# Kernel tuning notes

Measured on AMD Instinct MI355X. Metric: run time of the kernel, lower is better.

The kernel has to match this reference:

```python
import jax, jax.numpy as jnp
import numpy as np

EPS = 1e-5

def rmsnorm(x, weight, eps=EPS):
    var = jnp.mean(x * x, axis=-1, keepdims=True)
    return x * jax.lax.rsqrt(var + eps) * weight

def activation_quant(x):
    # per-token absmax int8 quantization (BitNet b1.58)
    scale = 127.0 / jnp.clip(jnp.max(jnp.abs(x), axis=-1, keepdims=True), 1e-5, None)
    return jnp.clip(jnp.round(x * scale), -128, 127) / scale

def weight_quant(w):
    # ternary absmean quantization
    scale = 1.0 / jnp.clip(jnp.mean(jnp.abs(w)), 1e-5, None)
    return jnp.clip(jnp.round(w * scale), -1, 1) / scale

def bitlinear(x, w):
    # forward math of BitLinear (STE only matters for backward)
    xq = activation_quant(x)
    wq = weight_quant(w)
    return jnp.einsum('bsh,oh->bso', xq, wq)

def setup_inputs() -> dict:
    key = jax.random.key(0)
    k1, k2, k3 = jax.random.split(key, 3)
    B, S, H, F = 4, 2048, 2048, 5632
    x = jax.random.normal(k1, (B, S, H), dtype=jnp.float32)
    w_gate_up = jax.random.normal(k2, (2 * F, H), dtype=jnp.float32) * 0.02
    w_down = jax.random.normal(k3, (H, F), dtype=jnp.float32) * 0.02
    norm_weight = jnp.ones((H,), dtype=jnp.float32)
    return {"x": x, "w_gate_up": w_gate_up, "w_down": w_down, "norm_weight": norm_weight}

def reference(x, w_gate_up, w_down, norm_weight):
    x_norm = rmsnorm(x, norm_weight)
    gate_up = bitlinear(x_norm, w_gate_up)          # [B,S,2F]
    gate, up = jnp.split(gate_up, 2, axis=-1)
    hidden = jnp.square(jax.nn.relu(gate)) * up      # relu(gate)**2 * up
    return bitlinear(hidden, w_down)                 # [B,S,H]
```

## Files before the change

### kernel.cpp

```cpp
#include <hip/hip_runtime.h>
#include <stdint.h>

typedef __attribute__((ext_vector_type(4))) float f32x4;
typedef __attribute__((ext_vector_type(4))) int i32x4;

#define ROWS  8192
#define H     2048
#define F     5632
#define N1    11264
#define NW1   23068672
#define NW2   11534336

__device__ __forceinline__ void gload16(const void* g, void* l) {
  __builtin_amdgcn_global_load_lds((const __attribute__((address_space(1))) void*)g,
                                   (__attribute__((address_space(3))) void*)l, 16, 0, 0);
}

__global__ void leaf_abs(const float* __restrict__ w, float* __restrict__ leaves) {
  int L = blockIdx.x * 256 + threadIdx.x;
  const f32x4* a4 = (const f32x4*)(w + (size_t)L * 88);
  f32x4 u0 = a4[0], u1 = a4[1];
  float r0 = fabsf(u0.x), r1 = fabsf(u0.y), r2 = fabsf(u0.z), r3 = fabsf(u0.w);
  float r4 = fabsf(u1.x), r5 = fabsf(u1.y), r6 = fabsf(u1.z), r7 = fabsf(u1.w);
  #pragma unroll
  for (int it = 1; it <= 10; ++it) {
    f32x4 p0 = a4[2*it], p1 = a4[2*it+1];
    r0 = __fadd_rn(r0, fabsf(p0.x)); r1 = __fadd_rn(r1, fabsf(p0.y));
    r2 = __fadd_rn(r2, fabsf(p0.z)); r3 = __fadd_rn(r3, fabsf(p0.w));
    r4 = __fadd_rn(r4, fabsf(p1.x)); r5 = __fadd_rn(r5, fabsf(p1.y));
    r6 = __fadd_rn(r6, fabsf(p1.z)); r7 = __fadd_rn(r7, fabsf(p1.w));
  }
  leaves[L] = __fadd_rn(__fadd_rn(__fadd_rn(r0,r1), __fadd_rn(r2,r3)),
                        __fadd_rn(__fadd_rn(r4,r5), __fadd_rn(r6,r7)));
}

__global__ void tree_l1(const float* __restrict__ leaves, float* __restrict__ partials) {
  __shared__ float sm[256];
  int tid = threadIdx.x;
  const float* b = leaves + (size_t)blockIdx.x * 1024 + (size_t)tid * 4;
  sm[tid] = __fadd_rn(__fadd_rn(b[0], b[1]), __fadd_rn(b[2], b[3]));
  __syncthreads();
  for (int s = 1; s < 256; s <<= 1) {
    if ((tid & (2*s-1)) == 0) sm[tid] = __fadd_rn(sm[tid], sm[tid+s]);
    __syncthreads();
  }
  if (tid == 0) partials[blockIdx.x] = sm[0];
}

__global__ void tree_final(const float* __restrict__ p1, const float* __restrict__ p2,
                           double* __restrict__ dsc, float* __restrict__ fsc) {
  __shared__ float sm[256];
  __shared__ float tot1s;
  int tid = threadIdx.x;
  sm[tid] = p1[tid];
  __syncthreads();
  for (int s = 1; s < 256; s <<= 1) {
    if ((tid & (2*s-1)) == 0) sm[tid] = __fadd_rn(sm[tid], sm[tid+s]);
    __syncthreads();
  }
  if (tid == 0) tot1s = sm[0];
  __syncthreads();
  sm[tid] = (tid < 128) ? p2[tid] : 0.0f;
  __syncthreads();
  for (int s = 1; s < 256; s <<= 1) {
    if ((tid & (2*s-1)) == 0) sm[tid] = __fadd_rn(sm[tid], sm[tid+s]);
    __syncthreads();
  }
  if (tid == 0) {
    float tot2 = sm[0];
    float mean1 = (float)((double)tot1s / (double)NW1);
    float mean2 = (float)((double)tot2  / (double)NW2);
    mean2 = __uint_as_float(__float_as_uint(mean2) + 1u);
    float m1c = fmaxf(mean1, 1e-5f), m2c = fmaxf(mean2, 1e-5f);
    float sc1 = __fdiv_rn(1.0f, m1c);
    float sc2 = __fdiv_rn(1.0f, m2c);
    fsc[0] = sc1; fsc[1] = sc2;
    dsc[0] = (double)sc1;
    dsc[1] = (double)__fdiv_rn(1.0f, sc1);
    dsc[2] = (double)sc2;
    dsc[3] = (double)__fdiv_rn(1.0f, sc2);
  }
}

__device__ __forceinline__ int qw32(float x, float sc) {
  float r = rintf(__fmul_rn(x, sc));
  r = fminf(fmaxf(r, -1.0f), 1.0f);
  return (int)r;
}
__device__ __forceinline__ int qa32(float x, float sc) {
  float r = rintf(__fmul_rn(x, sc));
  r = fminf(fmaxf(r, -128.0f), 127.0f);
  return (int)r;
}

__global__ void quant_wgu(const float* __restrict__ w, int8_t* __restrict__ q,
                          const float* __restrict__ fsc) {
  float sc = fsc[0];
  int t = blockIdx.x * 256 + threadIdx.x;
  int row = t >> 9;
  int k4 = (t & 511) << 2;
  f32x4 v = *(const f32x4*)(w + ((size_t)row << 11) + k4);
  int nr = (row < F) ? (row << 1) : (((row - F) << 1) | 1);
  int b0 = qw32(v.x, sc), b1 = qw32(v.y, sc), b2 = qw32(v.z, sc), b3 = qw32(v.w, sc);
  unsigned pk = (b0 & 255) | ((b1 & 255) << 8) | ((b2 & 255) << 16) | ((b3 & 255) << 24);
  *(unsigned*)(q + ((size_t)nr << 11) + k4) = pk;
}

__global__ void quant_wd(const float* __restrict__ w, int8_t* __restrict__ q,
                         const float* __restrict__ fsc) {
  float sc = fsc[1];
  int t = blockIdx.x * 256 + threadIdx.x;
  int row = t / 1408;
  int k4 = (t - row * 1408) << 2;
  size_t off = (size_t)row * F + k4;
  f32x4 v = *(const f32x4*)(w + off);
  int b0 = qw32(v.x, sc), b1 = qw32(v.y, sc), b2 = qw32(v.z, sc), b3 = qw32(v.w, sc);
  unsigned pk = (b0 & 255) | ((b1 & 255) << 8) | ((b2 & 255) << 16) | ((b3 & 255) << 24);
  *(unsigned*)(q + off) = pk;
}

__launch_bounds__(256)
__global__ void rms_quant(const float* __restrict__ x, const float* __restrict__ nw,
                          int8_t* __restrict__ xq, double* __restrict__ ax) {
  int row = blockIdx.x, tid = threadIdx.x;
  const float* xr = x + ((size_t)row << 11);
  __shared__ float lsm[16];
  __shared__ float sm[4];
  __shared__ float bc;
  if (tid < 16) {
    const f32x4* a4 = (const f32x4*)(xr + tid * 128);
    f32x4 u0 = a4[0], u1 = a4[1];
    float r0 = __fmul_rn(u0.x,u0.x), r1 = __fmul_rn(u0.y,u0.y);
    float r2 = __fmul_rn(u0.z,u0.z), r3 = __fmul_rn(u0.w,u0.w);
    float r4 = __fmul_rn(u1.x,u1.x), r5 = __fmul_rn(u1.y,u1.y);
    float r6 = __fmul_rn(u1.z,u1.z), r7 = __fmul_rn(u1.w,u1.w);
    #pragma unroll
    for (int it = 1; it <= 15; ++it) {
      f32x4 p0 = a4[2*it], p1 = a4[2*it+1];
      r0 = __fadd_rn(r0, __fmul_rn(p0.x,p0.x)); r1 = __fadd_rn(r1, __fmul_rn(p0.y,p0.y));
      r2 = __fadd_rn(r2, __fmul_rn(p0.z,p0.z)); r3 = __fadd_rn(r3, __fmul_rn(p0.w,p0.w));
      r4 = __fadd_rn(r4, __fmul_rn(p1.x,p1.x)); r5 = __fadd_rn(r5, __fmul_rn(p1.y,p1.y));
      r6 = __fadd_rn(r6, __fmul_rn(p1.z,p1.z)); r7 = __fadd_rn(r7, __fmul_rn(p1.w,p1.w));
    }
    lsm[tid] = __fadd_rn(__fadd_rn(__fadd_rn(r0,r1), __fadd_rn(r2,r3)),
                         __fadd_rn(__fadd_rn(r4,r5), __fadd_rn(r6,r7)));
  }
  __syncthreads();
  if (tid == 0) {
    float q0 = __fadd_rn(lsm[0],lsm[1]),  q1 = __fadd_rn(lsm[2],lsm[3]);
    float q2 = __fadd_rn(lsm[4],lsm[5]),  q3 = __fadd_rn(lsm[6],lsm[7]);
    float q4 = __fadd_rn(lsm[8],lsm[9]),  q5 = __fadd_rn(lsm[10],lsm[11]);
    float q6 = __fadd_rn(lsm[12],lsm[13]), q7 = __fadd_rn(lsm[14],lsm[15]);
    float h0 = __fadd_rn(q0,q1), h1 = __fadd_rn(q2,q3);
    float h2 = __fadd_rn(q4,q5), h3 = __fadd_rn(q6,q7);
    float s = __fadd_rn(__fadd_rn(h0,h1), __fadd_rn(h2,h3));
    float varm = (float)((double)s / 2048.0);
    bc = __fdiv_rn(1.0f, __fsqrt_rn(__fadd_rn(varm, 1e-5f)));
  }
  __syncthreads();
  float rstd = bc;
  f32x4 v0 = *(const f32x4*)(xr + tid * 8);
  f32x4 v1 = *(const f32x4*)(xr + tid * 8 + 4);
  f32x4 w0 = *(const f32x4*)(nw + tid * 8);
  f32x4 w1 = *(const f32x4*)(nw + tid * 8 + 4);
  float xv[8] = {v0.x,v0.y,v0.z,v0.w,v1.x,v1.y,v1.z,v1.w};
  float wv[8] = {w0.x,w0.y,w0.z,w0.w,w1.x,w1.y,w1.z,w1.w};
  float xn[8];
  float am = 0.f;
  #pragma unroll
  for (int j = 0; j < 8; ++j) {
    xn[j] = __fmul_rn(__fmul_rn(xv[j], rstd), wv[j]);
    am = fmaxf(am, fabsf(xn[j]));
  }
  int lane = tid & 63, wid = tid >> 6;
  for (int off = 32; off; off >>= 1) am = fmaxf(am, __shfl_down(am, off));
  if (lane == 0) sm[wid] = am;
  __syncthreads();
  if (tid == 0) {
    float amax = fmaxf(fmaxf(sm[0], sm[1]), fmaxf(sm[2], sm[3]));
    float sc = __fdiv_rn(127.0f, fmaxf(amax, 1e-5f));
    bc = sc;
    ax[row] = 1.0 / (double)sc;
  }
  __syncthreads();
  float sc = bc;
  int q[8];
  #pragma unroll
  for (int j = 0; j < 8; ++j) q[j] = qa32(xn[j], sc);
  int2 pk;
  pk.x = (q[0] & 255) | ((q[1] & 255) << 8) | ((q[2] & 255) << 16) | ((q[3] & 255) << 24);
  pk.y = (q[4] & 255) | ((q[5] & 255) << 8) | ((q[6] & 255) << 16) | ((q[7] & 255) << 24);
  *(int2*)(xq + ((size_t)row << 11) + tid * 8) = pk;
}

__launch_bounds__(512)
__global__ void hid_quant(const float* __restrict__ h,
                          int8_t* __restrict__ hq, double* __restrict__ ah) {
  int row = blockIdx.x, tid = threadIdx.x;
  __shared__ float rowbuf[F];
  __shared__ float sm[8];
  __shared__ float bc;
  const float* hr = h + (size_t)row * F;
  float am = 0.f;
  for (int i = tid * 4; i < F; i += 2048) {
    f32x4 v = *(const f32x4*)(hr + i);
    *(f32x4*)(rowbuf + i) = v;
    am = fmaxf(am, fmaxf(fmaxf(fabsf(v.x), fabsf(v.y)), fmaxf(fabsf(v.z), fabsf(v.w))));
  }
  int lane = tid & 63, wid = tid >> 6;
  for (int off = 32; off; off >>= 1) am = fmaxf(am, __shfl_down(am, off));
  if (lane == 0) sm[wid] = am;
  __syncthreads();
  if (tid == 0) {
    float amax = fmaxf(fmaxf(fmaxf(sm[0], sm[1]), fmaxf(sm[2], sm[3])),
                       fmaxf(fmaxf(sm[4], sm[5]), fmaxf(sm[6], sm[7])));
    amax = fmaxf(amax, 1e-5f);
    float sc = __fdiv_rn(127.0f, amax);
    bc = sc;
    ah[row] = 1.0 / (double)sc;
  }
  __syncthreads();
  float sc = bc;
  int8_t* qr = hq + (size_t)row * F;
  for (int i = tid * 4; i < F; i += 2048) {
    float vx = rowbuf[i], vy = rowbuf[i+1], vz = rowbuf[i+2], vw = rowbuf[i+3];
    int b0 = qa32(vx, sc), b1 = qa32(vy, sc), b2 = qa32(vz, sc), b3 = qa32(vw, sc);
    unsigned pk = (b0 & 255) | ((b1 & 255) << 8) | ((b2 & 255) << 16) | ((b3 & 255) << 24);
    *(unsigned*)(qr + i) = pk;
  }
}

template <bool GATEUP, int TNC>
__launch_bounds__(512, 2)
__global__ void gemm_i8(const int8_t* __restrict__ A, const int8_t* __restrict__ B,
                        int K, const double* __restrict__ arow,
                        const double* __restrict__ dsc, int dqidx,
                        float* __restrict__ outp, int ldo) {
  __shared__ __align__(16) int8_t lsA[4][256 * 64];
  __shared__ __align__(16) int8_t lsB[4][256 * 64];
  int tid = threadIdx.x, wid = tid >> 6, lane = tid & 63;
  int cpx = gridDim.x >> 3;
  int nid = (blockIdx.x & 7) * cpx + (blockIdx.x >> 3);
  int m0 = (nid / TNC) * 256, n0 = (nid % TNC) * 256;
  int wr = wid >> 2, wc = wid & 3;
  i32x4 acc[8][4] = {};
  double dq = dsc[dqidx];
  int nk = K >> 6;
  int schunk = (lane & 3) ^ ((lane >> 3) & 3);
  const int8_t* aS = A + (size_t)(m0 + wid * 16 + (lane >> 2)) * K + (schunk << 4);
  const int8_t* bS = B + (size_t)(n0 + wid * 16 + (lane >> 2)) * K + (schunk << 4);
  size_t hstep = (size_t)128 * K;
  int rl = lane & 15;
  int ksw = (((lane >> 4) ^ ((rl >> 1) & 3)) << 4);

  #define STAGE_A(t,h) gload16(aS + (size_t)(t)*64 + (size_t)(h)*hstep, \
                               &lsA[(t)&3][((h)*128 + wid*16)*64])
  #define STAGE_B(t,h) gload16(bS + (size_t)(t)*64 + (size_t)(h)*hstep, \
                               &lsB[(t)&3][((h)*128 + wid*16)*64])

  STAGE_A(0,0); STAGE_B(0,0); STAGE_A(0,1); STAGE_B(0,1);
  STAGE_A(1,0); STAGE_B(1,0); STAGE_A(1,1); STAGE_B(1,1);
  STAGE_A(2,0); STAGE_B(2,0); STAGE_A(2,1); STAGE_B(2,1);
  asm volatile("s_waitcnt vmcnt(8)" ::: "memory");
  __builtin_amdgcn_s_barrier();

  for (int t = 0; t < nk; ++t) {
    const int8_t* bufA = lsA[t & 3];
    const int8_t* bufB = lsB[t & 3];
    bool pf = (t + 3 < nk);
    i32x4 a[8], b[4];
    #pragma unroll
    for (int m = 0; m < 4; ++m)
      a[m] = *(const i32x4*)&bufA[(wr * 128 + m * 16 + rl) * 64 + ksw];
    #pragma unroll
    for (int n = 0; n < 4; ++n)
      b[n] = *(const i32x4*)&bufB[(wc * 64 + n * 16 + rl) * 64 + ksw];
    if (pf) { STAGE_A(t + 3, 0); STAGE_A(t + 3, 1); }
    __builtin_amdgcn_s_barrier();
    __builtin_amdgcn_s_setprio(1);
    #pragma unroll
    for (int m = 0; m < 4; ++m)
      #pragma unroll
      for (int n = 0; n < 4; ++n)
        acc[m][n] = __builtin_amdgcn_mfma_i32_16x16x64_i8(a[m], b[n], acc[m][n], 0, 0, 0);
    __builtin_amdgcn_s_setprio(0);
    __builtin_amdgcn_s_barrier();
    #pragma unroll
    for (int m = 4; m < 8; ++m)
      a[m] = *(const i32x4*)&bufA[(wr * 128 + m * 16 + rl) * 64 + ksw];
    if (pf) { STAGE_B(t + 3, 0); STAGE_B(t + 3, 1); }
    if (t + 3 < nk)      asm volatile("s_waitcnt vmcnt(8)" ::: "memory");
    else if (t + 2 < nk) asm volatile("s_waitcnt vmcnt(4)" ::: "memory");
    else if (t + 1 < nk) asm volatile("s_waitcnt vmcnt(0)" ::: "memory");
    __builtin_amdgcn_s_barrier();
    __builtin_amdgcn_s_setprio(1);
    #pragma unroll
    for (int m = 4; m < 8; ++m)
      #pragma unroll
      for (int n = 0; n < 4; ++n)
        acc[m][n] = __builtin_amdgcn_mfma_i32_16x16x64_i8(a[m], b[n], acc[m][n], 0, 0, 0);
    __builtin_amdgcn_s_setprio(0);
    __builtin_amdgcn_s_barrier();
  }
  #undef STAGE_A
  #undef STAGE_B

  int rb0 = m0 + wr * 128 + ((lane >> 4) << 2);
  #pragma unroll
  for (int m = 0; m < 8; ++m) {
    double arv[4];
    #pragma unroll
    for (int j = 0; j < 4; ++j)
      arv[j] = arow[rb0 + m * 16 + j] * dq;
    if (GATEUP) {
      #pragma unroll
      for (int n = 0; n < 4; ++n) {
        int icol = n0 + wc * 64 + n * 16 + rl;
        #pragma unroll
        for (int j = 0; j < 4; ++j) {
          float vf = (float)((double)acc[m][n][j] * arv[j]);
          float of = __shfl_xor(vf, 1);
          if (!(lane & 1)) {
            float g = fmaxf(vf, 0.0f);
            float hh = __fmul_rn(__fmul_rn(g, g), of);
            outp[(size_t)(rb0 + m * 16 + j) * ldo + (icol >> 1)] = hh;
          }
        }
      }
    } else {
      #pragma unroll
      for (int n = 0; n < 4; ++n) {
        int col = n0 + wc * 64 + n * 16 + rl;
        #pragma unroll
        for (int j = 0; j < 4; ++j)
          outp[(size_t)(rb0 + m * 16 + j) * ldo + col] = (float)((double)acc[m][n][j] * arv[j]);
      }
    }
  }
}

extern "C" void kernel_launch(void* const* d_in, const int* in_sizes, int n_in,
                              void* d_out, int out_size, void* d_ws, size_t ws_size,
                              hipStream_t stream) {
  (void)in_sizes; (void)n_in; (void)out_size; (void)ws_size;
  const float* x   = (const float*)d_in[0];
  const float* wgu = (const float*)d_in[1];
  const float* wd  = (const float*)d_in[2];
  const float* nw  = (const float*)d_in[3];
  float* out = (float*)d_out;

  char* p = (char*)d_ws;
  double*   dsc     = (double*)(p + 0);
  float*    fsc     = (float*)(p + 64);
  float*    part1   = (float*)(p + 128);
  float*    part2   = (float*)(p + 1152);
  float*    leaves1 = (float*)(p + 2048);
  float*    leaves2 = (float*)(p + 1050624);
  double*   ax      = (double*)(p + 1574912);
  double*   ah      = (double*)(p + 1640448);
  int8_t*   xq      = (int8_t*)(p + 2097152);
  int8_t*   wqg     = (int8_t*)(p + 18874368);
  int8_t*   wqd     = (int8_t*)(p + 41943040);
  int8_t*   hq      = (int8_t*)(p + 53477376);
  float*    hidden  = (float*)(p + 99614720);

  leaf_abs<<<1024, 256, 0, stream>>>(wgu, leaves1);
  leaf_abs<<<512,  256, 0, stream>>>(wd,  leaves2);
  tree_l1<<<256, 256, 0, stream>>>(leaves1, part1);
  tree_l1<<<128, 256, 0, stream>>>(leaves2, part2);
  tree_final<<<1, 256, 0, stream>>>(part1, part2, dsc, fsc);
  quant_wgu<<<NW1 / 4 / 256, 256, 0, stream>>>(wgu, wqg, fsc);
  quant_wd<<<NW2 / 4 / 256, 256, 0, stream>>>(wd, wqd, fsc);
  rms_quant<<<ROWS, 256, 0, stream>>>(x, nw, xq, ax);
  gemm_i8<true, 44><<<(ROWS / 256) * (N1 / 256), 512, 0, stream>>>(
      xq, wqg, H, ax, dsc, 1, hidden, F);
  hid_quant<<<ROWS, 512, 0, stream>>>(hidden, hq, ah);
  gemm_i8<false, 8><<<(ROWS / 256) * (H / 256), 512, 0, stream>>>(
      hq, wqd, F, ah, dsc, 3, out, H);
}
```

Baseline: 482.6 us.

## Double-buffer B fragments in registers and cut barriers in int8 GEMM loop

Rewrites the int8 MFMA GEMM main loop as a two-way unrolled body. The B fragments for the next k-step are prefetched into a second register set while the current step's MFMAs run. All global-to-LDS prefetches for stage t+3 are issued at once, with a single vmcnt wait and two barriers per k-step instead of four. This is meant to cut synchronisation stalls and hide LDS read latency behind MFMA work. The cost is higher register pressure from the extra B fragment set, and the loop now assumes an even k-step count.

```diff
diff --git a/kernel.cpp b/kernel.cpp
--- a/kernel.cpp
+++ b/kernel.cpp
@@ -230,6 +230,47 @@
   }
 }
 
+#define ITER_BODY(T, BCUR, BNXT)                                              \
+  {                                                                           \
+    if ((T) + 3 < nk) {                                                       \
+      STAGE_A((T)+3,0); STAGE_A((T)+3,1); STAGE_B((T)+3,0); STAGE_B((T)+3,1); \
+      asm volatile("s_waitcnt vmcnt(4)" ::: "memory");                        \
+    } else if ((T) + 2 < nk) {                                                \
+      asm volatile("s_waitcnt vmcnt(0)" ::: "memory");                        \
+    }                                                                         \
+    __builtin_amdgcn_s_barrier();                                             \
+    const int8_t* bufA_ = lsA[(T) & 3];                                       \
+    const int8_t* bufB1_ = lsB[((T) + 1) & 3];                                \
+    _Pragma("unroll")                                                         \
+    for (int m = 0; m < 4; ++m)                                               \
+      a[m] = *(const i32x4*)&bufA_[(wr * 128 + m * 16 + rl) * 64 + ksw];      \
+    __builtin_amdgcn_s_setprio(1);                                            \
+    _Pragma("unroll")                                                         \
+    for (int m = 0; m < 4; ++m)                                               \
+      _Pragma("unroll")                                                       \
+      for (int n = 0; n < 4; ++n)                                             \
+        acc[m][n] = __builtin_amdgcn_mfma_i32_16x16x64_i8(a[m], BCUR[n],      \
+                                                          acc[m][n], 0, 0, 0);\
+    __builtin_amdgcn_s_setprio(0);                                            \
+    _Pragma("unroll")                                                         \
+    for (int m = 4; m < 8; ++m)                                               \
+      a[m] = *(const i32x4*)&bufA_[(wr * 128 + m * 16 + rl) * 64 + ksw];      \
+    if ((T) + 1 < nk) {                                                       \
+      _Pragma("unroll")                                                       \
+      for (int n = 0; n < 4; ++n)                                             \
+        BNXT[n] = *(const i32x4*)&bufB1_[(wc * 64 + n * 16 + rl) * 64 + ksw]; \
+    }                                                                         \
+    __builtin_amdgcn_s_setprio(1);                                            \
+    _Pragma("unroll")                                                         \
+    for (int m = 4; m < 8; ++m)                                               \
+      _Pragma("unroll")                                                       \
+      for (int n = 0; n < 4; ++n)                                             \
+        acc[m][n] = __builtin_amdgcn_mfma_i32_16x16x64_i8(a[m], BCUR[n],      \
+                                                          acc[m][n], 0, 0, 0);\
+    __builtin_amdgcn_s_setprio(0);                                            \
+    __builtin_amdgcn_s_barrier();                                             \
+  }
+
 template <bool GATEUP, int TNC>
 __launch_bounds__(512, 2)
 __global__ void gemm_i8(const int8_t* __restrict__ A, const int8_t* __restrict__ B,
@@ -261,46 +302,17 @@
   STAGE_A(0,0); STAGE_B(0,0); STAGE_A(0,1); STAGE_B(0,1);
   STAGE_A(1,0); STAGE_B(1,0); STAGE_A(1,1); STAGE_B(1,1);
   STAGE_A(2,0); STAGE_B(2,0); STAGE_A(2,1); STAGE_B(2,1);
-  asm volatile("s_waitcnt vmcnt(8)" ::: "memory");
+  asm volatile("s_waitcnt vmcnt(4)" ::: "memory");
   __builtin_amdgcn_s_barrier();
 
-  for (int t = 0; t < nk; ++t) {
-    const int8_t* bufA = lsA[t & 3];
-    const int8_t* bufB = lsB[t & 3];
-    bool pf = (t + 3 < nk);
-    i32x4 a[8], b[4];
-    #pragma unroll
-    for (int m = 0; m < 4; ++m)
-      a[m] = *(const i32x4*)&bufA[(wr * 128 + m * 16 + rl) * 64 + ksw];
-    #pragma unroll
-    for (int n = 0; n < 4; ++n)
-      b[n] = *(const i32x4*)&bufB[(wc * 64 + n * 16 + rl) * 64 + ksw];
-    if (pf) { STAGE_A(t + 3, 0); STAGE_A(t + 3, 1); }
-    __builtin_amdgcn_s_barrier();
-    __builtin_amdgcn_s_setprio(1);
-    #pragma unroll
-    for (int m = 0; m < 4; ++m)
-      #pragma unroll
-      for (int n = 0; n < 4; ++n)
-        acc[m][n] = __builtin_amdgcn_mfma_i32_16x16x64_i8(a[m], b[n], acc[m][n], 0, 0, 0);
-    __builtin_amdgcn_s_setprio(0);
-    __builtin_amdgcn_s_barrier();
-    #pragma unroll
-    for (int m = 4; m < 8; ++m)
-      a[m] = *(const i32x4*)&bufA[(wr * 128 + m * 16 + rl) * 64 + ksw];
-    if (pf) { STAGE_B(t + 3, 0); STAGE_B(t + 3, 1); }
-    if (t + 3 < nk)      asm volatile("s_waitcnt vmcnt(8)" ::: "memory");
-    else if (t + 2 < nk) asm volatile("s_waitcnt vmcnt(4)" ::: "memory");
-    else if (t + 1 < nk) asm volatile("s_waitcnt vmcnt(0)" ::: "memory");
-    __builtin_amdgcn_s_barrier();
-    __builtin_amdgcn_s_setprio(1);
-    #pragma unroll
-    for (int m = 4; m < 8; ++m)
-      #pragma unroll
-      for (int n = 0; n < 4; ++n)
-        acc[m][n] = __builtin_amdgcn_mfma_i32_16x16x64_i8(a[m], b[n], acc[m][n], 0, 0, 0);
-    __builtin_amdgcn_s_setprio(0);
-    __builtin_amdgcn_s_barrier();
+  i32x4 a[8], bA[4], bB[4];
+  #pragma unroll
+  for (int n = 0; n < 4; ++n)
+    bA[n] = *(const i32x4*)&lsB[0][(wc * 64 + n * 16 + rl) * 64 + ksw];
+
+  for (int t = 0; t < nk; t += 2) {
+    ITER_BODY(t,     bA, bB)
+    ITER_BODY(t + 1, bB, bA)
   }
   #undef STAGE_A
   #undef STAGE_B
```

New measurement: 556.9 us. +15.4%, slower.

## Shrink int8 GEMM tiles to 128x128 with 256-thread blocks

Applied to the files above, without the earlier changes.

The int8 GEMM tile drops from 256x256 with 8 waves to 128x128 with 4 waves. Each wave keeps a 64x64 accumulator, LDS per block shrinks to a quarter, and the grid grows to four times as many blocks. The split-phase A/B prefetch schedule is merged into one phase per k-step with a single barrier pair. This may raise occupancy and improve wave balance across CUs, but each block reuses its loaded data less, so global and LDS traffic per MFMA goes up.

```diff
diff --git a/kernel.cpp b/kernel.cpp
--- a/kernel.cpp
+++ b/kernel.cpp
@@ -231,51 +231,55 @@
 }
 
 template <bool GATEUP, int TNC>
-__launch_bounds__(512, 2)
+__launch_bounds__(256, 2)
 __global__ void gemm_i8(const int8_t* __restrict__ A, const int8_t* __restrict__ B,
                         int K, const double* __restrict__ arow,
                         const double* __restrict__ dsc, int dqidx,
                         float* __restrict__ outp, int ldo) {
-  __shared__ __align__(16) int8_t lsA[4][256 * 64];
-  __shared__ __align__(16) int8_t lsB[4][256 * 64];
+  __shared__ __align__(16) int8_t lsA[4][128 * 64];
+  __shared__ __align__(16) int8_t lsB[4][128 * 64];
   int tid = threadIdx.x, wid = tid >> 6, lane = tid & 63;
   int cpx = gridDim.x >> 3;
   int nid = (blockIdx.x & 7) * cpx + (blockIdx.x >> 3);
-  int m0 = (nid / TNC) * 256, n0 = (nid % TNC) * 256;
-  int wr = wid >> 2, wc = wid & 3;
-  i32x4 acc[8][4] = {};
+  int m0 = (nid / TNC) * 128, n0 = (nid % TNC) * 128;
+  int wr = wid >> 1, wc = wid & 1;
+  i32x4 acc[4][4] = {};
   double dq = dsc[dqidx];
   int nk = K >> 6;
   int schunk = (lane & 3) ^ ((lane >> 3) & 3);
   const int8_t* aS = A + (size_t)(m0 + wid * 16 + (lane >> 2)) * K + (schunk << 4);
   const int8_t* bS = B + (size_t)(n0 + wid * 16 + (lane >> 2)) * K + (schunk << 4);
-  size_t hstep = (size_t)128 * K;
+  size_t hstep = (size_t)64 * K;
   int rl = lane & 15;
   int ksw = (((lane >> 4) ^ ((rl >> 1) & 3)) << 4);
 
   #define STAGE_A(t,h) gload16(aS + (size_t)(t)*64 + (size_t)(h)*hstep, \
-                               &lsA[(t)&3][((h)*128 + wid*16)*64])
+                               &lsA[(t)&3][((h)*64 + wid*16)*64])
   #define STAGE_B(t,h) gload16(bS + (size_t)(t)*64 + (size_t)(h)*hstep, \
-                               &lsB[(t)&3][((h)*128 + wid*16)*64])
-
-  STAGE_A(0,0); STAGE_B(0,0); STAGE_A(0,1); STAGE_B(0,1);
-  STAGE_A(1,0); STAGE_B(1,0); STAGE_A(1,1); STAGE_B(1,1);
-  STAGE_A(2,0); STAGE_B(2,0); STAGE_A(2,1); STAGE_B(2,1);
+                               &lsB[(t)&3][((h)*64 + wid*16)*64])
+
+  STAGE_A(0,0); STAGE_A(0,1); STAGE_B(0,0); STAGE_B(0,1);
+  STAGE_A(1,0); STAGE_A(1,1); STAGE_B(1,0); STAGE_B(1,1);
+  STAGE_A(2,0); STAGE_A(2,1); STAGE_B(2,0); STAGE_B(2,1);
   asm volatile("s_waitcnt vmcnt(8)" ::: "memory");
   __builtin_amdgcn_s_barrier();
 
   for (int t = 0; t < nk; ++t) {
     const int8_t* bufA = lsA[t & 3];
     const int8_t* bufB = lsB[t & 3];
-    bool pf = (t + 3 < nk);
-    i32x4 a[8], b[4];
+    i32x4 a[4], b[4];
     #pragma unroll
     for (int m = 0; m < 4; ++m)
-      a[m] = *(const i32x4*)&bufA[(wr * 128 + m * 16 + rl) * 64 + ksw];
+      a[m] = *(const i32x4*)&bufA[(wr * 64 + m * 16 + rl) * 64 + ksw];
     #pragma unroll
     for (int n = 0; n < 4; ++n)
       b[n] = *(const i32x4*)&bufB[(wc * 64 + n * 16 + rl) * 64 + ksw];
-    if (pf) { STAGE_A(t + 3, 0); STAGE_A(t + 3, 1); }
+    if (t + 3 < nk) {
+      STAGE_A(t+3,0); STAGE_A(t+3,1); STAGE_B(t+3,0); STAGE_B(t+3,1);
+      asm volatile("s_waitcnt vmcnt(8)" ::: "memory");
+    } else if (t + 2 < nk) {
+      asm volatile("s_waitcnt vmcnt(0)" ::: "memory");
+    }
     __builtin_amdgcn_s_barrier();
     __builtin_amdgcn_s_setprio(1);
     #pragma unroll
@@ -285,29 +289,13 @@
         acc[m][n] = __builtin_amdgcn_mfma_i32_16x16x64_i8(a[m], b[n], acc[m][n], 0, 0, 0);
     __builtin_amdgcn_s_setprio(0);
     __builtin_amdgcn_s_barrier();
-    #pragma unroll
-    for (int m = 4; m < 8; ++m)
-      a[m] = *(const i32x4*)&bufA[(wr * 128 + m * 16 + rl) * 64 + ksw];
-    if (pf) { STAGE_B(t + 3, 0); STAGE_B(t + 3, 1); }
-    if (t + 3 < nk)      asm volatile("s_waitcnt vmcnt(8)" ::: "memory");
-    else if (t + 2 < nk) asm volatile("s_waitcnt vmcnt(4)" ::: "memory");
-    else if (t + 1 < nk) asm volatile("s_waitcnt vmcnt(0)" ::: "memory");
-    __builtin_amdgcn_s_barrier();
-    __builtin_amdgcn_s_setprio(1);
-    #pragma unroll
-    for (int m = 4; m < 8; ++m)
-      #pragma unroll
-      for (int n = 0; n < 4; ++n)
-        acc[m][n] = __builtin_amdgcn_mfma_i32_16x16x64_i8(a[m], b[n], acc[m][n], 0, 0, 0);
-    __builtin_amdgcn_s_setprio(0);
-    __builtin_amdgcn_s_barrier();
   }
   #undef STAGE_A
   #undef STAGE_B
 
-  int rb0 = m0 + wr * 128 + ((lane >> 4) << 2);
+  int rb0 = m0 + wr * 64 + ((lane >> 4) << 2);
   #pragma unroll
-  for (int m = 0; m < 8; ++m) {
+  for (int m = 0; m < 4; ++m) {
     double arv[4];
     #pragma unroll
     for (int j = 0; j < 4; ++j)
@@ -372,9 +360,9 @@
   quant_wgu<<<NW1 / 4 / 256, 256, 0, stream>>>(wgu, wqg, fsc);
   quant_wd<<<NW2 / 4 / 256, 256, 0, stream>>>(wd, wqd, fsc);
   rms_quant<<<ROWS, 256, 0, stream>>>(x, nw, xq, ax);
-  gemm_i8<true, 44><<<(ROWS / 256) * (N1 / 256), 512, 0, stream>>>(
+  gemm_i8<true, 88><<<(ROWS / 128) * (N1 / 128), 256, 0, stream>>>(
       xq, wqg, H, ax, dsc, 1, hidden, F);
   hid_quant<<<ROWS, 512, 0, stream>>>(hidden, hq, ah);
-  gemm_i8<false, 8><<<(ROWS / 256) * (H / 256), 512, 0, stream>>>(
+  gemm_i8<false, 16><<<(ROWS / 128) * (H / 128), 256, 0, stream>>>(
       hq, wqd, F, ah, dsc, 3, out, H);
 }
```

Result: slower. 549.7 us (+13.9%).

## Restructure int8 GEMM main loop to stage two K-tiles per barrier pair

Applied to the files above, without the earlier changes.

The K loop now steps two tiles at a time. Each iteration issues the global-to-LDS loads for the next two tiles, waits, and hits one barrier. It then runs all 8x4 MFMAs for two tiles back to back. The earlier version split each tile into half-A phases with four barriers per tile and a three-deep prefetch. The aim is to cut barrier count and the interleaving overhead. In exchange, prefetch distance drops to two tiles with two in flight, so load latency is less well hidden, and more A fragments are live in registers at once.

```diff
diff --git a/kernel.cpp b/kernel.cpp
--- a/kernel.cpp
+++ b/kernel.cpp
@@ -253,57 +253,61 @@
   int rl = lane & 15;
   int ksw = (((lane >> 4) ^ ((rl >> 1) & 3)) << 4);
 
-  #define STAGE_A(t,h) gload16(aS + (size_t)(t)*64 + (size_t)(h)*hstep, \
-                               &lsA[(t)&3][((h)*128 + wid*16)*64])
-  #define STAGE_B(t,h) gload16(bS + (size_t)(t)*64 + (size_t)(h)*hstep, \
-                               &lsB[(t)&3][((h)*128 + wid*16)*64])
-
-  STAGE_A(0,0); STAGE_B(0,0); STAGE_A(0,1); STAGE_B(0,1);
-  STAGE_A(1,0); STAGE_B(1,0); STAGE_A(1,1); STAGE_B(1,1);
-  STAGE_A(2,0); STAGE_B(2,0); STAGE_A(2,1); STAGE_B(2,1);
-  asm volatile("s_waitcnt vmcnt(8)" ::: "memory");
-  __builtin_amdgcn_s_barrier();
-
-  for (int t = 0; t < nk; ++t) {
-    const int8_t* bufA = lsA[t & 3];
-    const int8_t* bufB = lsB[t & 3];
-    bool pf = (t + 3 < nk);
-    i32x4 a[8], b[4];
-    #pragma unroll
-    for (int m = 0; m < 4; ++m)
-      a[m] = *(const i32x4*)&bufA[(wr * 128 + m * 16 + rl) * 64 + ksw];
-    #pragma unroll
-    for (int n = 0; n < 4; ++n)
-      b[n] = *(const i32x4*)&bufB[(wc * 64 + n * 16 + rl) * 64 + ksw];
-    if (pf) { STAGE_A(t + 3, 0); STAGE_A(t + 3, 1); }
+  #define STAGE_T(t) { \
+    gload16(aS + (size_t)(t)*64,         &lsA[(t)&3][(wid*16)*64]);        \
+    gload16(aS + (size_t)(t)*64 + hstep, &lsA[(t)&3][(128 + wid*16)*64]);  \
+    gload16(bS + (size_t)(t)*64,         &lsB[(t)&3][(wid*16)*64]);        \
+    gload16(bS + (size_t)(t)*64 + hstep, &lsB[(t)&3][(128 + wid*16)*64]); }
+
+  STAGE_T(0); STAGE_T(1);
+
+  for (int t = 0; t < nk; t += 2) {
+    if (t + 2 < nk) {
+      STAGE_T(t + 2); STAGE_T(t + 3);
+      asm volatile("s_waitcnt vmcnt(8)" ::: "memory");
+    } else {
+      asm volatile("s_waitcnt vmcnt(0)" ::: "memory");
+    }
     __builtin_amdgcn_s_barrier();
-    __builtin_amdgcn_s_setprio(1);
-    #pragma unroll
-    for (int m = 0; m < 4; ++m)
+    {
+      const int8_t* bufA = lsA[t & 3];
+      const int8_t* bufB = lsB[t & 3];
+      i32x4 a[8], b[4];
+      #pragma unroll
+      for (int m = 0; m < 8; ++m)
+        a[m] = *(const i32x4*)&bufA[(wr * 128 + m * 16 + rl) * 64 + ksw];
       #pragma unroll
       for (int n = 0; n < 4; ++n)
-        acc[m][n] = __builtin_amdgcn_mfma_i32_16x16x64_i8(a[m], b[n], acc[m][n], 0, 0, 0);
-    __builtin_amdgcn_s_setprio(0);
+        b[n] = *(const i32x4*)&bufB[(wc * 64 + n * 16 + rl) * 64 + ksw];
+      __builtin_amdgcn_s_setprio(1);
+      #pragma unroll
+      for (int m = 0; m < 8; ++m)
+        #pragma unroll
+        for (int n = 0; n < 4; ++n)
+          acc[m][n] = __builtin_amdgcn_mfma_i32_16x16x64_i8(a[m], b[n], acc[m][n], 0, 0, 0);
+      __builtin_amdgcn_s_setprio(0);
+    }
+    {
+      const int8_t* bufA = lsA[(t + 1) & 3];
+      const int8_t* bufB = lsB[(t + 1) & 3];
+      i32x4 a[8], b[4];
+      #pragma unroll
+      for (int m = 0; m < 8; ++m)
+        a[m] = *(const i32x4*)&bufA[(wr * 128 + m * 16 + rl) * 64 + ksw];
+      #pragma unroll
+      for (int n = 0; n < 4; ++n)
+        b[n] = *(const i32x4*)&bufB[(wc * 64 + n * 16 + rl) * 64 + ksw];
+      __builtin_amdgcn_s_setprio(1);
+      #pragma unroll
+      for (int m = 0; m < 8; ++m)
+        #pragma unroll
+        for (int n = 0; n < 4; ++n)
+          acc[m][n] = __builtin_amdgcn_mfma_i32_16x16x64_i8(a[m], b[n], acc[m][n], 0, 0, 0);
+      __builtin_amdgcn_s_setprio(0);
+    }
     __builtin_amdgcn_s_barrier();
-    #pragma unroll
-    for (int m = 4; m < 8; ++m)
-      a[m] = *(const i32x4*)&bufA[(wr * 128 + m * 16 + rl) * 64 + ksw];
-    if (pf) { STAGE_B(t + 3, 0); STAGE_B(t + 3, 1); }
-    if (t + 3 < nk)      asm volatile("s_waitcnt vmcnt(8)" ::: "memory");
-    else if (t + 2 < nk) asm volatile("s_waitcnt vmcnt(4)" ::: "memory");
-    else if (t + 1 < nk) asm volatile("s_waitcnt vmcnt(0)" ::: "memory");
-    __builtin_amdgcn_s_barrier();
-    __builtin_amdgcn_s_setprio(1);
-    #pragma unroll
-    for (int m = 4; m < 8; ++m)
-      #pragma unroll
-      for (int n = 0; n < 4; ++n)
-        acc[m][n] = __builtin_amdgcn_mfma_i32_16x16x64_i8(a[m], b[n], acc[m][n], 0, 0, 0);
-    __builtin_amdgcn_s_setprio(0);
-    __builtin_amdgcn_s_barrier();
-  }
-  #undef STAGE_A
-  #undef STAGE_B
+  }
+  #undef STAGE_T
 
   int rb0 = m0 + wr * 128 + ((lane >> 4) << 2);
   #pragma unroll
```

After: 529.5 us. 9.7% more time.
